# Kernel optimization log

Hardware: AMD Instinct MI355X
Metric: run time of the kernel (lower is better)

Reference implementation:

```python
import jax, jax.numpy as jnp
import numpy as np

N_NODES = 10000
N_EDGES = 100000
DIM = 768
NEG_SLOPE = 0.2  # PyG GATConv default


def gat_conv(x, src, dst, W, att_src, att_dst, bias, num_nodes):
    """Single-head PyG-style GATConv. src/dst already include self-loops."""
    h = x @ W                                  # [N, D]
    a_s = h @ att_src                          # [N]
    a_d = h @ att_dst                          # [N]
    e = jax.nn.leaky_relu(a_s[src] + a_d[dst], NEG_SLOPE)  # [E']
    # segment softmax over edges sharing the same destination node
    m = jax.ops.segment_max(e, dst, num_segments=num_nodes)  # [N]
    e = jnp.exp(e - m[dst])
    denom = jax.ops.segment_sum(e, dst, num_segments=num_nodes)  # [N]
    alpha = e / denom[dst]                     # [E']
    msg = alpha[:, None] * h[src]              # [E', D]
    out = jax.ops.segment_sum(msg, dst, num_segments=num_nodes)  # [N, D]
    return out + bias


def setup_inputs() -> dict:
    key = jax.random.key(0)
    ks = jax.random.split(key, 12)
    s = 1.0 / np.sqrt(DIM)
    inp = {
        "x": jax.random.normal(ks[0], (N_NODES, DIM), dtype=jnp.float32),
        "edge_index": jax.random.randint(ks[1], (2, N_EDGES), 0, N_NODES, dtype=jnp.int64),
        "W1": jax.random.normal(ks[2], (DIM, DIM), dtype=jnp.float32) * s,
        "att_src1": jax.random.normal(ks[3], (DIM,), dtype=jnp.float32) * s,
        "att_dst1": jax.random.normal(ks[4], (DIM,), dtype=jnp.float32) * s,
        "b1": jnp.zeros((DIM,), dtype=jnp.float32),
        "W2": jax.random.normal(ks[5], (DIM, DIM), dtype=jnp.float32) * s,
        "att_src2": jax.random.normal(ks[6], (DIM,), dtype=jnp.float32) * s,
        "att_dst2": jax.random.normal(ks[7], (DIM,), dtype=jnp.float32) * s,
        "b2": jnp.zeros((DIM,), dtype=jnp.float32),
    }
    return inp


def reference(x, edge_index, W1, att_src1, att_dst1, b1, W2, att_src2, att_dst2, b2):
    n = x.shape[0]
    # PyG GATConv default add_self_loops=True
    loops = jnp.arange(n, dtype=edge_index.dtype)
    src = jnp.concatenate([edge_index[0], loops])
    dst = jnp.concatenate([edge_index[1], loops])
    h = gat_conv(x, src, dst, W1, att_src1, att_dst1, b1, n)
    h = jax.nn.relu(h)
    # dropout p=0.0 in eval -> identity
    out = gat_conv(h, src, dst, W2, att_src2, att_dst2, b2, n)
    return out
```

## Files before the change

### kernel.cpp

```cpp
#include <hip/hip_runtime.h>

#define DIM 768
#define NEG_SLOPE 0.2f

typedef unsigned short ushort_t;
typedef short short8 __attribute__((ext_vector_type(8)));
typedef float floatx4 __attribute__((ext_vector_type(4)));

__device__ __forceinline__ ushort_t f32_to_bf16(float f) {
  unsigned int b = __float_as_uint(f);
  b += 0x7FFFu + ((b >> 16) & 1u);
  return (ushort_t)(b >> 16);
}
__device__ __forceinline__ float bf16_to_f32(ushort_t u) {
  return __uint_as_float(((unsigned int)u) << 16);
}
__device__ __forceinline__ float bf16lo(unsigned int u) {
  return __uint_as_float(u << 16);
}
__device__ __forceinline__ float bf16hi(unsigned int u) {
  return __uint_as_float(u & 0xFFFF0000u);
}
__device__ __forceinline__ unsigned int pack_bf16x2(float lo, float hi) {
  return ((unsigned int)f32_to_bf16(lo)) | (((unsigned int)f32_to_bf16(hi)) << 16);
}

__device__ __forceinline__ void gl2lds16(const ushort_t* g, ushort_t* l) {
  __builtin_amdgcn_global_load_lds(
      (const __attribute__((address_space(1))) void*)g,
      (__attribute__((address_space(3))) void*)l, 16, 0, 0);
}

__global__ __launch_bounds__(256)
void prep_kernel(const float* __restrict__ x, ushort_t* __restrict__ xb, int n4,
                 const float* __restrict__ W1, ushort_t* __restrict__ wT1,
                 const float* __restrict__ W2, ushort_t* __restrict__ wT2,
                 int* __restrict__ zbase, int nz) {
  int i = blockIdx.x * 256 + threadIdx.x;
  if (i < n4) {
    float4 v = ((const float4*)x)[i];
    ushort4 o;
    o.x = f32_to_bf16(v.x); o.y = f32_to_bf16(v.y);
    o.z = f32_to_bf16(v.z); o.w = f32_to_bf16(v.w);
    ((ushort4*)xb)[i] = o;
  }
  if (i < DIM * DIM) {
    int nrow = i / DIM;
    int k = i - nrow * DIM;
    wT1[i] = f32_to_bf16(W1[k * DIM + nrow]);
    wT2[i] = f32_to_bf16(W2[k * DIM + nrow]);
  }
  if (i < nz) zbase[i] = 0;
}

__global__ void hist_kernel(const int* __restrict__ ei, int* __restrict__ deg,
                            int E, int Etot) {
  int e = blockIdx.x * 256 + threadIdx.x;
  if (e >= Etot) return;
  int d = (e < E) ? ei[E + e] : (e - E);
  atomicAdd(&deg[d], 1);
}

__global__ __launch_bounds__(256)
void scan_kernel(const int* __restrict__ deg, int* __restrict__ rowstart,
                 int* __restrict__ cursor, int n, int etot) {
  __shared__ int sdeg[10240];
  __shared__ int part[256];
  int tid = threadIdx.x;
  for (int i = tid; i < n; i += 256) sdeg[i] = deg[i];
  __syncthreads();
  int chunk = ((n + 255) / 256) | 1;
  int lo = min(tid * chunk, n);
  int hi = min(lo + chunk, n);
  int s = 0;
  for (int i = lo; i < hi; ++i) s += sdeg[i];
  part[tid] = s;
  __syncthreads();
  for (int off = 1; off < 256; off <<= 1) {
    int v = part[tid];
    int add = (tid >= off) ? part[tid - off] : 0;
    __syncthreads();
    part[tid] = v + add;
    __syncthreads();
  }
  int run = (tid == 0) ? 0 : part[tid - 1];
  for (int i = lo; i < hi; ++i) {
    int d = sdeg[i];
    sdeg[i] = run;
    run += d;
  }
  __syncthreads();
  for (int i = tid; i < n; i += 256) {
    int v = sdeg[i];
    rowstart[i] = v;
    cursor[i] = v;
  }
  if (tid == 0) rowstart[n] = etot;
}

__global__ void fill_kernel(const int* __restrict__ ei, int* __restrict__ cursor,
                            int* __restrict__ col, int E, int Etot) {
  int e = blockIdx.x * 256 + threadIdx.x;
  if (e >= Etot) return;
  int s, d;
  if (e < E) { s = ei[e]; d = ei[E + e]; }
  else       { s = e - E; d = e - E; }
  int pos = atomicAdd(&cursor[d], 1);
  col[pos] = s;
}

__global__ __launch_bounds__(256)
void gemm_kernel(const ushort_t* __restrict__ A, const ushort_t* __restrict__ Bt,
                 const float* __restrict__ att_s, const float* __restrict__ att_d,
                 float* __restrict__ a_s, float* __restrict__ a_d,
                 ushort_t* __restrict__ Hb, int M) {
  const int K = DIM;
  __shared__ __align__(16) ushort_t As[128 * 64];
  __shared__ __align__(16) ushort_t Bs[128 * 64];
  int tid = threadIdx.x;
  int m0 = blockIdx.x * 128, n0 = blockIdx.y * 128;
  int wave = tid >> 6, lane = tid & 63;
  int wm = (wave & 1) * 64, wn = (wave >> 1) * 64;
  int quad = lane >> 4, l16 = lane & 15;

  floatx4 acc[4][4];
  const floatx4 fzero = {0.f, 0.f, 0.f, 0.f};
#pragma unroll
  for (int i = 0; i < 4; ++i)
#pragma unroll
    for (int j = 0; j < 4; ++j) acc[i][j] = fzero;

  int lr = lane >> 3, lc = lane & 7;
  const ushort_t* gA[4];
  const ushort_t* gB[4];
  ushort_t* lA[4];
  ushort_t* lB[4];
#pragma unroll
  for (int t = 0; t < 4; ++t) {
    int r = t * 32 + wave * 8 + lr;
    int g = lc ^ (r & 7);
    gA[t] = A + (size_t)min(m0 + r, M - 1) * K + g * 8;
    gB[t] = Bt + (size_t)(n0 + r) * K + g * 8;
    lA[t] = As + (t * 32 + wave * 8) * 64;
    lB[t] = Bs + (t * 32 + wave * 8) * 64;
  }

  for (int k0 = 0; k0 < K; k0 += 64) {
#pragma unroll
    for (int t = 0; t < 4; ++t) {
      gl2lds16(gA[t] + k0, lA[t]);
      gl2lds16(gB[t] + k0, lB[t]);
    }
    __syncthreads();

#pragma unroll
    for (int h = 0; h < 2; ++h) {
      short8 af[4], bfr[4];
#pragma unroll
      for (int i = 0; i < 4; ++i) {
        int ra = wm + i * 16 + l16;
        af[i] = *(const short8*)(As + ra * 64 + ((((h << 2) | quad)) ^ (ra & 7)) * 8);
        int rb = wn + i * 16 + l16;
        bfr[i] = *(const short8*)(Bs + rb * 64 + ((((h << 2) | quad)) ^ (rb & 7)) * 8);
      }
#pragma unroll
      for (int i = 0; i < 4; ++i)
#pragma unroll
        for (int j = 0; j < 4; ++j)
          acc[i][j] = __builtin_amdgcn_mfma_f32_16x16x32_bf16(af[i], bfr[j], acc[i][j], 0, 0, 0);
    }
    __syncthreads();
  }

  float avs[4], avd[4];
#pragma unroll
  for (int j = 0; j < 4; ++j) {
    int c = n0 + wn + j * 16 + l16;
    avs[j] = att_s[c];
    avd[j] = att_d[c];
  }

#pragma unroll
  for (int i = 0; i < 4; ++i) {
#pragma unroll
    for (int r = 0; r < 4; ++r) {
      int row = m0 + wm + i * 16 + quad * 4 + r;
      bool valid = row < M;
      float pvs = 0.f, pvd = 0.f;
#pragma unroll
      for (int j = 0; j < 4; ++j) {
        float v = acc[i][j][r];
        if (valid) Hb[(size_t)row * DIM + n0 + wn + j * 16 + l16] = f32_to_bf16(v);
        pvs = fmaf(v, avs[j], pvs);
        pvd = fmaf(v, avd[j], pvd);
      }
#pragma unroll
      for (int off = 1; off < 16; off <<= 1) {
        pvs += __shfl_xor(pvs, off, 64);
        pvd += __shfl_xor(pvd, off, 64);
      }
      if (valid && l16 == 0) {
        atomicAdd(a_s + row, pvs);
        atomicAdd(a_d + row, pvd);
      }
    }
  }
}

__global__ __launch_bounds__(256)
void aggregate_kernel(const ushort_t* __restrict__ h, const float* __restrict__ a_s,
                      const float* __restrict__ a_d, const int* __restrict__ rowstart,
                      const int* __restrict__ col, const float* __restrict__ bias,
                      float* __restrict__ out_f32, ushort_t* __restrict__ out_bf16,
                      int relu_mode, int N) {
  int wave = threadIdx.x >> 6, lane = threadIdx.x & 63;
  int node = blockIdx.x * 4 + wave;
  if (node >= N) return;
  int start = rowstart[node], end = rowstart[node + 1];
  float ad = a_d[node];

  float vmax = -3.4e38f;
  for (int e = start + lane; e < end; e += 64) {
    float v = a_s[col[e]] + ad;
    v = (v > 0.f) ? v : NEG_SLOPE * v;
    vmax = fmaxf(vmax, v);
  }
#pragma unroll
  for (int off = 32; off > 0; off >>= 1) vmax = fmaxf(vmax, __shfl_xor(vmax, off, 64));

  float ssum = 0.f;
  for (int e = start + lane; e < end; e += 64) {
    float v = a_s[col[e]] + ad;
    v = (v > 0.f) ? v : NEG_SLOPE * v;
    ssum += __expf(v - vmax);
  }
#pragma unroll
  for (int off = 32; off > 0; off >>= 1) ssum += __shfl_xor(ssum, off, 64);
  float inv = 1.f / ssum;

  float acc8[8];
  float acc4[4];
#pragma unroll
  for (int k = 0; k < 8; ++k) acc8[k] = 0.f;
#pragma unroll
  for (int k = 0; k < 4; ++k) acc4[k] = 0.f;

  for (int base = start; base < end; base += 64) {
    int e = base + lane;
    float al = 0.f;
    int sc = 0;
    if (e < end) {
      sc = col[e];
      float v = a_s[sc] + ad;
      v = (v > 0.f) ? v : NEG_SLOPE * v;
      al = __expf(v - vmax) * inv;
    }
    int cnt = min(64, end - base);
    for (int j = 0; j < cnt; ++j) {
      float w = __shfl(al, j, 64);
      int s = __shfl(sc, j, 64);
      const ushort_t* hr = h + (size_t)s * DIM;
      uint4 u = *(const uint4*)(hr + lane * 8);
      ushort4 t = *(const ushort4*)(hr + 512 + lane * 4);
      acc8[0] = fmaf(w, bf16lo(u.x), acc8[0]);
      acc8[1] = fmaf(w, bf16hi(u.x), acc8[1]);
      acc8[2] = fmaf(w, bf16lo(u.y), acc8[2]);
      acc8[3] = fmaf(w, bf16hi(u.y), acc8[3]);
      acc8[4] = fmaf(w, bf16lo(u.z), acc8[4]);
      acc8[5] = fmaf(w, bf16hi(u.z), acc8[5]);
      acc8[6] = fmaf(w, bf16lo(u.w), acc8[6]);
      acc8[7] = fmaf(w, bf16hi(u.w), acc8[7]);
      acc4[0] = fmaf(w, bf16_to_f32(t.x), acc4[0]);
      acc4[1] = fmaf(w, bf16_to_f32(t.y), acc4[1]);
      acc4[2] = fmaf(w, bf16_to_f32(t.z), acc4[2]);
      acc4[3] = fmaf(w, bf16_to_f32(t.w), acc4[3]);
    }
  }

  size_t ob = (size_t)node * DIM;
  int c8 = lane * 8, c4 = 512 + lane * 4;
  float4 b0 = *(const float4*)(bias + c8);
  float4 b1 = *(const float4*)(bias + c8 + 4);
  float4 b2 = *(const float4*)(bias + c4);
  float o[12];
  o[0] = acc8[0] + b0.x; o[1] = acc8[1] + b0.y;
  o[2] = acc8[2] + b0.z; o[3] = acc8[3] + b0.w;
  o[4] = acc8[4] + b1.x; o[5] = acc8[5] + b1.y;
  o[6] = acc8[6] + b1.z; o[7] = acc8[7] + b1.w;
  o[8] = acc4[0] + b2.x; o[9] = acc4[1] + b2.y;
  o[10] = acc4[2] + b2.z; o[11] = acc4[3] + b2.w;
  if (relu_mode) {
#pragma unroll
    for (int k = 0; k < 12; ++k) o[k] = fmaxf(o[k], 0.f);
    uint4 s0;
    s0.x = pack_bf16x2(o[0], o[1]);
    s0.y = pack_bf16x2(o[2], o[3]);
    s0.z = pack_bf16x2(o[4], o[5]);
    s0.w = pack_bf16x2(o[6], o[7]);
    *(uint4*)(out_bf16 + ob + c8) = s0;
    uint2 s1;
    s1.x = pack_bf16x2(o[8], o[9]);
    s1.y = pack_bf16x2(o[10], o[11]);
    *(uint2*)(out_bf16 + ob + c4) = s1;
  } else {
    *(float4*)(out_f32 + ob + c8) = make_float4(o[0], o[1], o[2], o[3]);
    *(float4*)(out_f32 + ob + c8 + 4) = make_float4(o[4], o[5], o[6], o[7]);
    *(float4*)(out_f32 + ob + c4) = make_float4(o[8], o[9], o[10], o[11]);
  }
}

extern "C" void kernel_launch(void* const* d_in, const int* in_sizes, int n_in,
                              void* d_out, int out_size, void* d_ws, size_t ws_size,
                              hipStream_t stream) {
  const float* x   = (const float*)d_in[0];
  const int*   ei  = (const int*)d_in[1];
  const float* W1  = (const float*)d_in[2];
  const float* as1 = (const float*)d_in[3];
  const float* ad1 = (const float*)d_in[4];
  const float* b1  = (const float*)d_in[5];
  const float* W2  = (const float*)d_in[6];
  const float* as2 = (const float*)d_in[7];
  const float* ad2 = (const float*)d_in[8];
  const float* b2  = (const float*)d_in[9];

  const int N = in_sizes[0] / DIM;
  const int E = in_sizes[1] / 2;
  const int Etot = E + N;

  char* p = (char*)d_ws;
  auto alloc = [&](size_t bytes) {
    char* q = p;
    p += (bytes + 255) & ~(size_t)255;
    return q;
  };
  ushort_t* Hb     = (ushort_t*)alloc((size_t)N * DIM * 2);
  ushort_t* xb     = (ushort_t*)alloc((size_t)N * DIM * 2);
  ushort_t* wT1    = (ushort_t*)alloc((size_t)DIM * DIM * 2);
  ushort_t* wT2    = (ushort_t*)alloc((size_t)DIM * DIM * 2);
  int*      zbase  = (int*)alloc((size_t)5 * N * 4);
  int*      deg    = zbase;
  float*    a_s1   = (float*)(zbase + N);
  float*    a_d1   = (float*)(zbase + 2 * N);
  float*    a_s2   = (float*)(zbase + 3 * N);
  float*    a_d2   = (float*)(zbase + 4 * N);
  int*      rowst  = (int*)alloc((size_t)(N + 1) * 4);
  int*      cursor = (int*)alloc((size_t)N * 4);
  int*      col    = (int*)alloc((size_t)Etot * 4);

  prep_kernel<<<(N * DIM / 4 + 255) / 256, 256, 0, stream>>>(
      x, xb, N * DIM / 4, W1, wT1, W2, wT2, zbase, 5 * N);
  hist_kernel<<<(Etot + 255) / 256, 256, 0, stream>>>(ei, deg, E, Etot);
  scan_kernel<<<1, 256, 0, stream>>>(deg, rowst, cursor, N, Etot);
  fill_kernel<<<(Etot + 255) / 256, 256, 0, stream>>>(ei, cursor, col, E, Etot);

  dim3 ggrid((N + 127) / 128, DIM / 128);

  gemm_kernel<<<ggrid, 256, 0, stream>>>(xb, wT1, as1, ad1, a_s1, a_d1, Hb, N);
  aggregate_kernel<<<(N + 3) / 4, 256, 0, stream>>>(Hb, a_s1, a_d1, rowst, col, b1,
                                                    nullptr, xb, 1, N);
  gemm_kernel<<<ggrid, 256, 0, stream>>>(xb, wT2, as2, ad2, a_s2, a_d2, Hb, N);
  aggregate_kernel<<<(N + 3) / 4, 256, 0, stream>>>(Hb, a_s2, a_d2, rowst, col, b2,
                                                    (float*)d_out, nullptr, 0, N);
}
```

Measured before the change: 233.4 us.

## Retile GEMM with XCD-aware mapping, tiled weight transpose, prefetch gathers, wider scan

```diff
diff --git a/kernel.cpp b/kernel.cpp
--- a/kernel.cpp
+++ b/kernel.cpp
@@ -35,22 +35,48 @@
 void prep_kernel(const float* __restrict__ x, ushort_t* __restrict__ xb, int n4,
                  const float* __restrict__ W1, ushort_t* __restrict__ wT1,
                  const float* __restrict__ W2, ushort_t* __restrict__ wT2,
-                 int* __restrict__ zbase, int nz) {
-  int i = blockIdx.x * 256 + threadIdx.x;
-  if (i < n4) {
-    float4 v = ((const float4*)x)[i];
-    ushort4 o;
-    o.x = f32_to_bf16(v.x); o.y = f32_to_bf16(v.y);
-    o.z = f32_to_bf16(v.z); o.w = f32_to_bf16(v.w);
-    ((ushort4*)xb)[i] = o;
-  }
-  if (i < DIM * DIM) {
-    int nrow = i / DIM;
-    int k = i - nrow * DIM;
-    wT1[i] = f32_to_bf16(W1[k * DIM + nrow]);
-    wT2[i] = f32_to_bf16(W2[k * DIM + nrow]);
-  }
-  if (i < nz) zbase[i] = 0;
+                 int* __restrict__ zbase, int nz4) {
+  __shared__ ushort_t tile[64][65];
+  int b = blockIdx.x;
+  int t = threadIdx.x;
+  if (b < 288) {
+    int mat = b / 144;
+    int ti = b - mat * 144;
+    int tr = (ti / 12) * 64;
+    int tc = (ti % 12) * 64;
+    const float* W = mat ? W2 : W1;
+    ushort_t* wT = mat ? wT2 : wT1;
+    int lr = t >> 4, lc4 = (t & 15) * 4;
+#pragma unroll
+    for (int p = 0; p < 4; ++p) {
+      int row = lr + p * 16;
+      float4 v = *(const float4*)(W + (size_t)(tr + row) * DIM + tc + lc4);
+      tile[row][lc4 + 0] = f32_to_bf16(v.x);
+      tile[row][lc4 + 1] = f32_to_bf16(v.y);
+      tile[row][lc4 + 2] = f32_to_bf16(v.z);
+      tile[row][lc4 + 3] = f32_to_bf16(v.w);
+    }
+    __syncthreads();
+    int n = t & 63, kb = (t >> 6) * 16;
+    ushort_t tmp[16];
+#pragma unroll
+    for (int i = 0; i < 16; ++i) tmp[i] = tile[kb + i][n];
+    ushort_t* dst = wT + (size_t)(tc + n) * DIM + tr + kb;
+    *(uint4*)(dst) = *(const uint4*)(&tmp[0]);
+    *(uint4*)(dst + 8) = *(const uint4*)(&tmp[8]);
+  } else {
+    int i = (b - 288) * 256 + t;
+    if (i < n4) {
+      float4 v = ((const float4*)x)[i];
+      ushort4 o;
+      o.x = f32_to_bf16(v.x); o.y = f32_to_bf16(v.y);
+      o.z = f32_to_bf16(v.z); o.w = f32_to_bf16(v.w);
+      ((ushort4*)xb)[i] = o;
+    }
+    if (i < nz4) {
+      ((uint4*)zbase)[i] = make_uint4(0, 0, 0, 0);
+    }
+  }
 }
 
 __global__ void hist_kernel(const int* __restrict__ ei, int* __restrict__ deg,
@@ -61,22 +87,22 @@
   atomicAdd(&deg[d], 1);
 }
 
-__global__ __launch_bounds__(256)
+__global__ __launch_bounds__(1024)
 void scan_kernel(const int* __restrict__ deg, int* __restrict__ rowstart,
                  int* __restrict__ cursor, int n, int etot) {
   __shared__ int sdeg[10240];
-  __shared__ int part[256];
+  __shared__ int part[1024];
   int tid = threadIdx.x;
-  for (int i = tid; i < n; i += 256) sdeg[i] = deg[i];
+  for (int i = tid; i < n; i += 1024) sdeg[i] = deg[i];
   __syncthreads();
-  int chunk = ((n + 255) / 256) | 1;
+  int chunk = ((n + 1023) / 1024) | 1;
   int lo = min(tid * chunk, n);
   int hi = min(lo + chunk, n);
   int s = 0;
   for (int i = lo; i < hi; ++i) s += sdeg[i];
   part[tid] = s;
   __syncthreads();
-  for (int off = 1; off < 256; off <<= 1) {
+  for (int off = 1; off < 1024; off <<= 1) {
     int v = part[tid];
     int add = (tid >= off) ? part[tid - off] : 0;
     __syncthreads();
@@ -90,7 +116,7 @@
     run += d;
   }
   __syncthreads();
-  for (int i = tid; i < n; i += 256) {
+  for (int i = tid; i < n; i += 1024) {
     int v = sdeg[i];
     rowstart[i] = v;
     cursor[i] = v;
@@ -113,68 +139,80 @@
 void gemm_kernel(const ushort_t* __restrict__ A, const ushort_t* __restrict__ Bt,
                  const float* __restrict__ att_s, const float* __restrict__ att_d,
                  float* __restrict__ a_s, float* __restrict__ a_d,
-                 ushort_t* __restrict__ Hb, int M) {
+                 ushort_t* __restrict__ Hb, int M, int MBLK) {
   const int K = DIM;
-  __shared__ __align__(16) ushort_t As[128 * 64];
+  __shared__ __align__(16) ushort_t As[64 * 64];
   __shared__ __align__(16) ushort_t Bs[128 * 64];
+  int b = blockIdx.x;
+  int x = b & 7, sidx = b >> 3;
+  int m_local = sidx / 6, nblk = sidx - m_local * 6;
+  int mblk = x * MBLK + m_local;
+  if (mblk * 64 >= M) return;
+  int m0 = mblk * 64, n0 = nblk * 128;
   int tid = threadIdx.x;
-  int m0 = blockIdx.x * 128, n0 = blockIdx.y * 128;
   int wave = tid >> 6, lane = tid & 63;
-  int wm = (wave & 1) * 64, wn = (wave >> 1) * 64;
   int quad = lane >> 4, l16 = lane & 15;
-
-  floatx4 acc[4][4];
+  int wn = wave * 32;
+
+  floatx4 acc[4][2];
   const floatx4 fzero = {0.f, 0.f, 0.f, 0.f};
 #pragma unroll
   for (int i = 0; i < 4; ++i)
 #pragma unroll
-    for (int j = 0; j < 4; ++j) acc[i][j] = fzero;
+    for (int j = 0; j < 2; ++j) acc[i][j] = fzero;
 
   int lr = lane >> 3, lc = lane & 7;
-  const ushort_t* gA[4];
+  const ushort_t* gA[2];
   const ushort_t* gB[4];
-  ushort_t* lA[4];
+  ushort_t* lA[2];
   ushort_t* lB[4];
+#pragma unroll
+  for (int t = 0; t < 2; ++t) {
+    int r = t * 32 + wave * 8 + lr;
+    int g = lc ^ (r & 7);
+    gA[t] = A + (size_t)min(m0 + r, M - 1) * K + g * 8;
+    lA[t] = As + (t * 32 + wave * 8) * 64;
+  }
 #pragma unroll
   for (int t = 0; t < 4; ++t) {
     int r = t * 32 + wave * 8 + lr;
     int g = lc ^ (r & 7);
-    gA[t] = A + (size_t)min(m0 + r, M - 1) * K + g * 8;
     gB[t] = Bt + (size_t)(n0 + r) * K + g * 8;
-    lA[t] = As + (t * 32 + wave * 8) * 64;
     lB[t] = Bs + (t * 32 + wave * 8) * 64;
   }
 
   for (int k0 = 0; k0 < K; k0 += 64) {
 #pragma unroll
-    for (int t = 0; t < 4; ++t) {
-      gl2lds16(gA[t] + k0, lA[t]);
-      gl2lds16(gB[t] + k0, lB[t]);
-    }
+    for (int t = 0; t < 2; ++t) gl2lds16(gA[t] + k0, lA[t]);
+#pragma unroll
+    for (int t = 0; t < 4; ++t) gl2lds16(gB[t] + k0, lB[t]);
     __syncthreads();
 
 #pragma unroll
     for (int h = 0; h < 2; ++h) {
-      short8 af[4], bfr[4];
+      short8 af[4], bfr[2];
 #pragma unroll
       for (int i = 0; i < 4; ++i) {
-        int ra = wm + i * 16 + l16;
+        int ra = i * 16 + l16;
         af[i] = *(const short8*)(As + ra * 64 + ((((h << 2) | quad)) ^ (ra & 7)) * 8);
-        int rb = wn + i * 16 + l16;
-        bfr[i] = *(const short8*)(Bs + rb * 64 + ((((h << 2) | quad)) ^ (rb & 7)) * 8);
+      }
+#pragma unroll
+      for (int j = 0; j < 2; ++j) {
+        int rb = wn + j * 16 + l16;
+        bfr[j] = *(const short8*)(Bs + rb * 64 + ((((h << 2) | quad)) ^ (rb & 7)) * 8);
       }
 #pragma unroll
       for (int i = 0; i < 4; ++i)
 #pragma unroll
-        for (int j = 0; j < 4; ++j)
+        for (int j = 0; j < 2; ++j)
           acc[i][j] = __builtin_amdgcn_mfma_f32_16x16x32_bf16(af[i], bfr[j], acc[i][j], 0, 0, 0);
     }
     __syncthreads();
   }
 
-  float avs[4], avd[4];
-#pragma unroll
-  for (int j = 0; j < 4; ++j) {
+  float avs[2], avd[2];
+#pragma unroll
+  for (int j = 0; j < 2; ++j) {
     int c = n0 + wn + j * 16 + l16;
     avs[j] = att_s[c];
     avd[j] = att_d[c];
@@ -183,13 +221,13 @@
 #pragma unroll
   for (int i = 0; i < 4; ++i) {
 #pragma unroll
-    for (int r = 0; r < 4; ++r) {
-      int row = m0 + wm + i * 16 + quad * 4 + r;
+    for (int r2 = 0; r2 < 4; ++r2) {
+      int row = m0 + i * 16 + quad * 4 + r2;
       bool valid = row < M;
       float pvs = 0.f, pvd = 0.f;
 #pragma unroll
-      for (int j = 0; j < 4; ++j) {
-        float v = acc[i][j][r];
+      for (int j = 0; j < 2; ++j) {
+        float v = acc[i][j][r2];
         if (valid) Hb[(size_t)row * DIM + n0 + wn + j * 16 + l16] = f32_to_bf16(v);
         pvs = fmaf(v, avs[j], pvs);
         pvd = fmaf(v, avd[j], pvd);
@@ -256,12 +294,22 @@
       al = __expf(v - vmax) * inv;
     }
     int cnt = min(64, end - base);
+    float w = __shfl(al, 0, 64);
+    int s = __shfl(sc, 0, 64);
+    const ushort_t* hr = h + (size_t)s * DIM;
+    uint4 u = *(const uint4*)(hr + lane * 8);
+    ushort4 t4 = *(const ushort4*)(hr + 512 + lane * 4);
     for (int j = 0; j < cnt; ++j) {
-      float w = __shfl(al, j, 64);
-      int s = __shfl(sc, j, 64);
-      const ushort_t* hr = h + (size_t)s * DIM;
-      uint4 u = *(const uint4*)(hr + lane * 8);
-      ushort4 t = *(const ushort4*)(hr + 512 + lane * 4);
+      float wn_ = 0.f;
+      uint4 un;
+      ushort4 tn;
+      if (j + 1 < cnt) {
+        wn_ = __shfl(al, j + 1, 64);
+        int sn = __shfl(sc, j + 1, 64);
+        const ushort_t* hrn = h + (size_t)sn * DIM;
+        un = *(const uint4*)(hrn + lane * 8);
+        tn = *(const ushort4*)(hrn + 512 + lane * 4);
+      }
       acc8[0] = fmaf(w, bf16lo(u.x), acc8[0]);
       acc8[1] = fmaf(w, bf16hi(u.x), acc8[1]);
       acc8[2] = fmaf(w, bf16lo(u.y), acc8[2]);
@@ -270,10 +318,11 @@
       acc8[5] = fmaf(w, bf16hi(u.z), acc8[5]);
       acc8[6] = fmaf(w, bf16lo(u.w), acc8[6]);
       acc8[7] = fmaf(w, bf16hi(u.w), acc8[7]);
-      acc4[0] = fmaf(w, bf16_to_f32(t.x), acc4[0]);
-      acc4[1] = fmaf(w, bf16_to_f32(t.y), acc4[1]);
-      acc4[2] = fmaf(w, bf16_to_f32(t.z), acc4[2]);
-      acc4[3] = fmaf(w, bf16_to_f32(t.w), acc4[3]);
+      acc4[0] = fmaf(w, bf16_to_f32(t4.x), acc4[0]);
+      acc4[1] = fmaf(w, bf16_to_f32(t4.y), acc4[1]);
+      acc4[2] = fmaf(w, bf16_to_f32(t4.z), acc4[2]);
+      acc4[3] = fmaf(w, bf16_to_f32(t4.w), acc4[3]);
+      if (j + 1 < cnt) { w = wn_; u = un; t4 = tn; }
     }
   }
 
@@ -337,7 +386,7 @@
   ushort_t* xb     = (ushort_t*)alloc((size_t)N * DIM * 2);
   ushort_t* wT1    = (ushort_t*)alloc((size_t)DIM * DIM * 2);
   ushort_t* wT2    = (ushort_t*)alloc((size_t)DIM * DIM * 2);
-  int*      zbase  = (int*)alloc((size_t)5 * N * 4);
+  int*      zbase  = (int*)alloc((size_t)5 * N * 4 + 16);
   int*      deg    = zbase;
   float*    a_s1   = (float*)(zbase + N);
   float*    a_d1   = (float*)(zbase + 2 * N);
@@ -347,18 +396,24 @@
   int*      cursor = (int*)alloc((size_t)N * 4);
   int*      col    = (int*)alloc((size_t)Etot * 4);
 
-  prep_kernel<<<(N * DIM / 4 + 255) / 256, 256, 0, stream>>>(
-      x, xb, N * DIM / 4, W1, wT1, W2, wT2, zbase, 5 * N);
+  int n4 = N * DIM / 4;
+  int nz4 = (5 * N + 3) / 4;
+  int prep_blocks = 288 + (n4 + 255) / 256;
+  prep_kernel<<<prep_blocks, 256, 0, stream>>>(x, xb, n4, W1, wT1, W2, wT2,
+                                               zbase, nz4);
   hist_kernel<<<(Etot + 255) / 256, 256, 0, stream>>>(ei, deg, E, Etot);
-  scan_kernel<<<1, 256, 0, stream>>>(deg, rowst, cursor, N, Etot);
+  scan_kernel<<<1, 1024, 0, stream>>>(deg, rowst, cursor, N, Etot);
   fill_kernel<<<(Etot + 255) / 256, 256, 0, stream>>>(ei, cursor, col, E, Etot);
 
-  dim3 ggrid((N + 127) / 128, DIM / 128);
-
-  gemm_kernel<<<ggrid, 256, 0, stream>>>(xb, wT1, as1, ad1, a_s1, a_d1, Hb, N);
-  aggregate_kernel<<<(N + 3) / 4, 256, 0, stream>>>(Hb, a_s1, a_d1, rowst, col, b1,
-                                                    nullptr, xb, 1, N);
-  gemm_kernel<<<ggrid, 256, 0, stream>>>(xb, wT2, as2, ad2, a_s2, a_d2, Hb, N);
-  aggregate_kernel<<<(N + 3) / 4, 256, 0, stream>>>(Hb, a_s2, a_d2, rowst, col, b2,
-                                                    (float*)d_out, nullptr, 0, N);
-}
+  int MB = (N + 63) / 64;
+  int MBLK = (MB + 7) / 8;
+  int gemm_blocks = 8 * MBLK * 6;
+  int agg_blocks = (N + 3) / 4;
+
+  gemm_kernel<<<gemm_blocks, 256, 0, stream>>>(xb, wT1, as1, ad1, a_s1, a_d1, Hb, N, MBLK);
+  aggregate_kernel<<<agg_blocks, 256, 0, stream>>>(Hb, a_s1, a_d1, rowst, col, b1,
+                                                   nullptr, xb, 1, N);
+  gemm_kernel<<<gemm_blocks, 256, 0, stream>>>(xb, wT2, as2, ad2, a_s2, a_d2, Hb, N, MBLK);
+  aggregate_kernel<<<agg_blocks, 256, 0, stream>>>(Hb, a_s2, a_d2, rowst, col, b2,
+                                                   (float*)d_out, nullptr, 0, N);
+}
```

Result: no change. 231.9 us (-0.6%).
